# Kernel tuning notes

Hardware: AMD Instinct MI355X
Metric: run time of the kernel (lower is better)

Reference implementation:

```python
import jax, jax.numpy as jnp
import numpy as np

DIM = 1024; DEPTH = 6; HEADS = 16; DH = 64; NF = 16; VOCAB = 20000; B = 4; N = 1024
INNER = HEADS * DH
FF_INNER = int(DIM * 4 * 2 / 3)  # GEGLU inner dim = 2730


def _ln(x, g):
    # torch F.layer_norm with beta=0 buffer, eps=1e-5
    m = x.mean(-1, keepdims=True)
    v = ((x - m) ** 2).mean(-1, keepdims=True)
    return (x - m) / jnp.sqrt(v + 1e-5) * g


def _attn(x, ctx, mask, ln_g, Wq, Wkv, Wo):
    # faithful: LayerNorm applied to x (queries); context, if given, used raw for k/v
    xn = _ln(x, ln_g)
    kv_x = xn if ctx is None else ctx
    b, i, _ = x.shape
    j = kv_x.shape[1]
    q = (xn @ Wq).reshape(b, i, HEADS, DH) * (DH ** -0.5)
    k, v = jnp.split(kv_x @ Wkv, 2, axis=-1)
    k = k.reshape(b, j, HEADS, DH)
    v = v.reshape(b, j, HEADS, DH)
    sim = jnp.einsum('bihd,bjhd->bhij', q, k)
    sim = jnp.where(mask, sim, -jnp.finfo(sim.dtype).max)
    attn = jax.nn.softmax(sim, axis=-1)
    out = jnp.einsum('bhij,bjhd->bihd', attn, v).reshape(b, i, INNER)
    return out @ Wo


def _closs(a, b, ls):
    # CLIP-style ContrastiveLossWithTemperature
    an = a / jnp.linalg.norm(a, axis=-1, keepdims=True)
    bn = b / jnp.linalg.norm(b, axis=-1, keepdims=True)
    logits = jnp.exp(ls) * (an @ bn.T)
    lab = jnp.arange(a.shape[0])
    la = -jax.nn.log_softmax(logits, axis=-1)[lab, lab].mean()
    lb = -jax.nn.log_softmax(logits.T, axis=-1)[lab, lab].mean()
    return (la + lb) * 0.5


def setup_inputs() -> dict:
    key = jax.random.key(0)
    ks = jax.random.split(key, 16)
    rn = lambda k, s: jax.random.normal(k, s, jnp.float32) * 0.02
    return {
        'spliced_data': jax.random.normal(ks[0], (B, N), jnp.float32),
        'spliced_index': jax.random.randint(ks[1], (B, N), 0, VOCAB),
        'emb': rn(ks[2], (VOCAB, DIM)),
        'fusion_tokens': jax.random.normal(ks[3], (NF, DIM), jnp.float32),
        'return_tokens': jax.random.normal(ks[4], (2, DIM), jnp.float32),
        'ln1_g': jnp.ones((DEPTH, DIM), jnp.float32),
        'Wq': rn(ks[5], (DEPTH, DIM, INNER)),
        'Wkv': rn(ks[6], (DEPTH, DIM, 2 * INNER)),
        'Wo': rn(ks[7], (DEPTH, INNER, DIM)),
        'ln2_g': jnp.ones((DEPTH, DIM), jnp.float32),
        'Wff1': rn(ks[8], (DEPTH, DIM, 2 * FF_INNER)),
        'Wff2': rn(ks[9], (DEPTH, FF_INNER, DIM)),
        'norm_g': jnp.ones((DIM,), jnp.float32),
        'pool_ln_g': jnp.ones((DIM,), jnp.float32),
        'pWq': rn(ks[10], (DIM, INNER)),
        'pWkv': rn(ks[11], (DIM, 2 * INNER)),
        'pWo': rn(ks[12], (INNER, DIM)),
        'logit_scale_c': jnp.float32(np.log(1.0 / 0.07)),
        'logit_scale_f': jnp.float32(np.log(1.0 / 0.07)),
    }


def reference(spliced_data, spliced_index, emb, fusion_tokens, return_tokens,
              ln1_g, Wq, Wkv, Wo, ln2_g, Wff1, Wff2, norm_g,
              pool_ln_g, pWq, pWkv, pWo, logit_scale_c, logit_scale_f):
    b = spliced_data.shape[0]
    # BioZorroEncoder: value-weighted embedding lookup
    spliced_tokens = emb[spliced_index] * spliced_data[..., None]  # [b, N, DIM]
    tokens = jnp.concatenate(
        [spliced_tokens, jnp.broadcast_to(fusion_tokens, (b, NF, DIM))], axis=1)
    tt = jnp.concatenate([jnp.zeros((N,), jnp.int32), jnp.ones((NF,), jnp.int32)])
    # spliced attends spliced; fusion attends everything
    zmask = (tt[:, None] == tt[None, :]) | (tt[:, None] == 1)

    def body(t, p):
        l1, wq, wkv, wo, l2, w1, w2 = p
        t = _attn(t, None, zmask, l1, wq, wkv, wo) + t
        h = _ln(t, l2) @ w1
        xh, gate = jnp.split(h, 2, axis=-1)
        t = (jax.nn.gelu(gate, approximate=False) * xh) @ w2 + t
        return t, None

    tokens, _ = jax.lax.scan(body, tokens, (ln1_g, Wq, Wkv, Wo, ln2_g, Wff1, Wff2))
    tokens = _ln(tokens, norm_g)

    rtt = jnp.array([0, 1], jnp.int32)
    pm0 = rtt[:, None] == tt[None, :]
    # faithful to source operator precedence: (pm0 | rtt) == GLOBAL(2) -> all False
    pm = (pm0.astype(jnp.int32) | rtt[:, None]) == 2

    ret = jnp.broadcast_to(return_tokens, (b, 2, DIM))
    pooled = _attn(ret, tokens, pm, pool_ln_g, pWq, pWkv, pWo) + ret

    spliced = pooled[:, 0]
    fusion = pooled[:, 1]
    loss = _closs(spliced, spliced, logit_scale_c) + _closs(spliced, fusion, logit_scale_f)
    return loss
```

## Files before the change

kernel.cpp:

```cpp
#include <hip/hip_runtime.h>

typedef unsigned short u16;
typedef unsigned long long u64;
typedef __attribute__((ext_vector_type(8))) short short8;
typedef __attribute__((ext_vector_type(4))) float f32x4;

__device__ __forceinline__ u16 f2b(float f) {
  union { float f; unsigned u; } x; x.f = f;
  unsigned r = x.u + 0x7fffu + ((x.u >> 16) & 1u);
  return (u16)(r >> 16);
}
__device__ __forceinline__ float b2f(u16 h) {
  union { unsigned u; float f; } x; x.u = ((unsigned)h) << 16;
  return x.f;
}
__device__ __forceinline__ void gld16(const void* g, void* l) {
  __builtin_amdgcn_global_load_lds(
      (__attribute__((address_space(1))) const void*)g,
      (__attribute__((address_space(3))) void*)l, 16, 0, 0);
}

__global__ __launch_bounds__(256) void embed_k(
    const float* __restrict__ data, const int* __restrict__ idx,
    const float* __restrict__ emb, const float* __restrict__ fus,
    float* __restrict__ t) {
  int row = blockIdx.x;
  int b = row / 1040, n = row % 1040;
  int tid = threadIdx.x;
  const float4* src;
  float sc = 1.f;
  if (n < 1024) {
    int e = idx[b * 1024 + n];
    sc = data[b * 1024 + n];
    src = (const float4*)(emb + (long)e * 1024);
  } else {
    src = (const float4*)(fus + (long)(n - 1024) * 1024);
  }
  float4 v = src[tid];
  v.x *= sc; v.y *= sc; v.z *= sc; v.w *= sc;
  ((float4*)(t + (long)row * 1024))[tid] = v;
}

__global__ __launch_bounds__(256) void wtrans5_k(
    const float* __restrict__ sWq, const float* __restrict__ sWkv,
    const float* __restrict__ sWo, const float* __restrict__ sW1,
    const float* __restrict__ sW2,
    u16* __restrict__ dQkvT, u16* __restrict__ dWoT,
    u16* __restrict__ dF1T, u16* __restrict__ dF2T) {
  int id = blockIdx.x;
  const float* src; u16* dst; int K, N, Kpad, nx; float sc = 1.f;
  if (id < 1024)       { src = sWq;  dst = dQkvT;             K = 1024; N = 1024; Kpad = 1024; nx = 32; sc = 0.125f; }
  else if (id < 3072)  { id -= 1024; src = sWkv; dst = dQkvT + 1024 * 1024; K = 1024; N = 2048; Kpad = 1024; nx = 64; }
  else if (id < 4096)  { id -= 3072; src = sWo;  dst = dWoT;  K = 1024; N = 1024; Kpad = 1024; nx = 32; }
  else if (id < 9600)  { id -= 4096; src = sW1;  dst = dF1T;  K = 1024; N = 5460; Kpad = 1024; nx = 172; }
  else                 { id -= 9600; src = sW2;  dst = dF2T;  K = 2730; N = 1024; Kpad = 2752; nx = 32; }
  int n0 = (id % nx) * 32, k0 = (id / nx) * 32;
  __shared__ float tile[32][33];
  int x = threadIdx.x & 31, y = threadIdx.x >> 5;
#pragma unroll
  for (int i = 0; i < 4; i++) {
    int k = k0 + y + i * 8, n = n0 + x;
    tile[y + i * 8][x] = (k < K && n < N) ? src[(long)k * N + n] * sc : 0.f;
  }
  __syncthreads();
#pragma unroll
  for (int i = 0; i < 4; i++) {
    int n = n0 + y + i * 8, k = k0 + x;
    dst[(long)n * Kpad + k] = f2b(tile[x][y + i * 8]);
  }
}

__global__ __launch_bounds__(256) void ln_k(
    const float* __restrict__ t, const float* __restrict__ g,
    u16* __restrict__ xn) {
  int row = blockIdx.x, tid = threadIdx.x;
  int wave = tid >> 6, lane = tid & 63;
  float4 v = ((const float4*)(t + (long)row * 1024))[tid];
  float s = v.x + v.y + v.z + v.w;
#pragma unroll
  for (int o = 32; o > 0; o >>= 1) s += __shfl_xor(s, o, 64);
  __shared__ float r1[4], r2[4];
  if (lane == 0) r1[wave] = s;
  __syncthreads();
  float mean = (r1[0] + r1[1] + r1[2] + r1[3]) * (1.f / 1024.f);
  float dx = v.x - mean, dy = v.y - mean, dz = v.z - mean, dw = v.w - mean;
  float q = dx * dx + dy * dy + dz * dz + dw * dw;
#pragma unroll
  for (int o = 32; o > 0; o >>= 1) q += __shfl_xor(q, o, 64);
  if (lane == 0) r2[wave] = q;
  __syncthreads();
  float var = (r2[0] + r2[1] + r2[2] + r2[3]) * (1.f / 1024.f);
  float inv = rsqrtf(var + 1e-5f);
  float4 gv = ((const float4*)g)[tid];
  u64 pack = (u64)f2b(dx * inv * gv.x)
           | ((u64)f2b(dy * inv * gv.y) << 16)
           | ((u64)f2b(dz * inv * gv.z) << 32)
           | ((u64)f2b(dw * inv * gv.w) << 48);
  *(u64*)(xn + (long)row * 1024 + tid * 4) = pack;
}

__global__ __launch_bounds__(256) void lnred_k(
    float* __restrict__ t, const float* __restrict__ p0, const float* __restrict__ p1,
    const float* __restrict__ g, u16* __restrict__ xn) {
  int row = blockIdx.x, tid = threadIdx.x;
  int wave = tid >> 6, lane = tid & 63;
  long base = (long)row * 1024;
  float4 v = ((const float4*)(t + base))[tid];
  float4 a = ((const float4*)(p0 + base))[tid];
  float4 bq = ((const float4*)(p1 + base))[tid];
  v.x += a.x + bq.x; v.y += a.y + bq.y; v.z += a.z + bq.z; v.w += a.w + bq.w;
  ((float4*)(t + base))[tid] = v;
  float s = v.x + v.y + v.z + v.w;
#pragma unroll
  for (int o = 32; o > 0; o >>= 1) s += __shfl_xor(s, o, 64);
  __shared__ float r1[4], r2[4];
  if (lane == 0) r1[wave] = s;
  __syncthreads();
  float mean = (r1[0] + r1[1] + r1[2] + r1[3]) * (1.f / 1024.f);
  float dx = v.x - mean, dy = v.y - mean, dz = v.z - mean, dw = v.w - mean;
  float q = dx * dx + dy * dy + dz * dz + dw * dw;
#pragma unroll
  for (int o = 32; o > 0; o >>= 1) q += __shfl_xor(q, o, 64);
  if (lane == 0) r2[wave] = q;
  __syncthreads();
  float var = (r2[0] + r2[1] + r2[2] + r2[3]) * (1.f / 1024.f);
  float inv = rsqrtf(var + 1e-5f);
  float4 gv = ((const float4*)g)[tid];
  u64 pack = (u64)f2b(dx * inv * gv.x)
           | ((u64)f2b(dy * inv * gv.y) << 16)
           | ((u64)f2b(dz * inv * gv.z) << 32)
           | ((u64)f2b(dw * inv * gv.w) << 48);
  *(u64*)(xn + base + tid * 4) = pack;
}

__global__ __launch_bounds__(256) void redrow_k(
    float* __restrict__ t, const float* __restrict__ p0, const float* __restrict__ p1,
    float* __restrict__ rowm, float* __restrict__ rinv) {
  int row = blockIdx.x, tid = threadIdx.x;
  int wave = tid >> 6, lane = tid & 63;
  long base = (long)row * 1024;
  float4 v = ((const float4*)(t + base))[tid];
  float4 a = ((const float4*)(p0 + base))[tid];
  float4 bq = ((const float4*)(p1 + base))[tid];
  v.x += a.x + bq.x; v.y += a.y + bq.y; v.z += a.z + bq.z; v.w += a.w + bq.w;
  ((float4*)(t + base))[tid] = v;
  float s = v.x + v.y + v.z + v.w;
#pragma unroll
  for (int o = 32; o > 0; o >>= 1) s += __shfl_xor(s, o, 64);
  __shared__ float r1[4], r2[4];
  if (lane == 0) r1[wave] = s;
  __syncthreads();
  float mean = (r1[0] + r1[1] + r1[2] + r1[3]) * (1.f / 1024.f);
  float dx = v.x - mean, dy = v.y - mean, dz = v.z - mean, dw = v.w - mean;
  float q = dx * dx + dy * dy + dz * dz + dw * dw;
#pragma unroll
  for (int o = 32; o > 0; o >>= 1) q += __shfl_xor(q, o, 64);
  if (lane == 0) r2[wave] = q;
  __syncthreads();
  if (tid == 0) {
    float var = (r2[0] + r2[1] + r2[2] + r2[3]) * (1.f / 1024.f);
    rowm[row] = mean;
    rinv[row] = rsqrtf(var + 1e-5f);
  }
}

__global__ __launch_bounds__(256) void gemm_bt(
    const u16* __restrict__ A, int lda,
    const u16* __restrict__ Bt, int ldb,
    void* __restrict__ C, int ldc,
    int K, int mode, int gx, int ns, long pstride, u16* __restrict__ vt) {
  __shared__ u16 As[3][128 * 32];
  __shared__ u16 Bs[3][128 * 32];
  int tid = threadIdx.x;
  int wave = tid >> 6, lane = tid & 63;
  int col = lane & 15, grp = lane >> 4;
  int nwg = gridDim.x;
  int id = blockIdx.x;
  int q = nwg >> 3, r = nwg & 7;
  int xcd = id & 7, off = id >> 3;
  int wgid = (xcd < r ? xcd * (q + 1) : r * (q + 1) + (xcd - r) * q) + off;
  int tiles = nwg / ns;
  int ksp = wgid / tiles;
  int rem = wgid % tiles;
  int bm = rem % gx, bn = rem / gx;
  int nst = K >> 5;
  int k0 = ((nst * ksp) / ns) << 5;
  int k1 = ((nst * (ksp + 1)) / ns) << 5;
  int sr = wave * 16 + (lane >> 2);
  int sk = ((lane & 3) ^ ((lane >> 3) & 3)) * 8;
  const u16* aSrc = A + ((long)bm * 128 + sr) * lda + sk;
  const u16* bSrc = Bt + ((long)bn * 128 + sr) * ldb + sk;
  int wm = (wave >> 1) * 64, wn = (wave & 1) * 64;
  f32x4 acc[4][4] = {};

#define GSTAGE(buf, kt) do { \
    _Pragma("unroll") \
    for (int qq = 0; qq < 2; qq++) { \
      gld16(aSrc + (kt) + (long)qq * 64 * lda, &As[buf][wave * 512 + qq * 2048]); \
      gld16(bSrc + (kt) + (long)qq * 64 * ldb, &Bs[buf][wave * 512 + qq * 2048]); \
    } } while (0)

  GSTAGE(0, k0);
  if (k0 + 32 < k1) GSTAGE(1, k0 + 32);
  int cur = 0;
  int slot = (grp ^ ((col >> 1) & 3)) * 8;
  for (int kt = k0; kt < k1; kt += 32) {
    if (kt + 64 < k1) {
      int nb = cur + 2; if (nb >= 3) nb -= 3;
      GSTAGE(nb, kt + 64);
      asm volatile("s_waitcnt vmcnt(8)" ::: "memory");
    } else if (kt + 32 < k1) {
      asm volatile("s_waitcnt vmcnt(4)" ::: "memory");
    } else {
      asm volatile("s_waitcnt vmcnt(0)" ::: "memory");
    }
    __builtin_amdgcn_s_barrier();
    __builtin_amdgcn_sched_barrier(0);
    short8 af[4], bfv[4];
#pragma unroll
    for (int m = 0; m < 4; m++)
      af[m] = *(const short8*)&As[cur][(wm + m * 16 + col) * 32 + slot];
#pragma unroll
    for (int n = 0; n < 4; n++)
      bfv[n] = *(const short8*)&Bs[cur][(wn + n * 16 + col) * 32 + slot];
    __builtin_amdgcn_s_setprio(1);
#pragma unroll
    for (int m = 0; m < 4; m++)
#pragma unroll
      for (int n = 0; n < 4; n++)
        acc[m][n] = __builtin_amdgcn_mfma_f32_16x16x32_bf16(af[m], bfv[n], acc[m][n], 0, 0, 0);
    __builtin_amdgcn_s_setprio(0);
    __builtin_amdgcn_s_barrier();
    __builtin_amdgcn_sched_barrier(0);
    cur = (cur == 2) ? 0 : cur + 1;
  }
#undef GSTAGE
  long r0 = (long)bm * 128 + wm + grp * 4;
  int c0 = bn * 128 + wn + col;
  if (mode != 1) {
    u16* Cb = (u16*)C;
#pragma unroll
    for (int m = 0; m < 4; m++)
#pragma unroll
      for (int n = 0; n < 4; n++)
#pragma unroll
        for (int rr = 0; rr < 4; rr++)
          Cb[(r0 + m * 16 + rr) * ldc + c0 + n * 16] = f2b(acc[m][n][rr]);
    if (mode == 2 && bn >= 16) {
#pragma unroll
      for (int m = 0; m < 4; m++) {
        long row = r0 + m * 16;
        if (row < 4160) {
          int bidx = (int)(row / 1040);
          int j = (int)(row - (long)bidx * 1040);
#pragma unroll
          for (int n = 0; n < 4; n++) {
            int d = c0 + n * 16 - 2048;
            u64 pack = (u64)f2b(acc[m][n][0])
                     | ((u64)f2b(acc[m][n][1]) << 16)
                     | ((u64)f2b(acc[m][n][2]) << 32)
                     | ((u64)f2b(acc[m][n][3]) << 48);
            *(u64*)(vt + ((long)(bidx * 16 + (d >> 6)) * 64 + (d & 63)) * 1040 + j) = pack;
          }
        }
      }
    }
  } else {
    float* Cf = (float*)C + (long)ksp * pstride;
#pragma unroll
    for (int m = 0; m < 4; m++)
#pragma unroll
      for (int n = 0; n < 4; n++)
#pragma unroll
        for (int rr = 0; rr < 4; rr++)
          Cf[(r0 + m * 16 + rr) * ldc + c0 + n * 16] = acc[m][n][rr];
  }
}

__global__ __launch_bounds__(256) void attn_k(
    const u16* __restrict__ qkv, const u16* __restrict__ vt,
    u16* __restrict__ out) {
  int nwg = gridDim.x;
  int id = blockIdx.x;
  int q = nwg >> 3, r = nwg & 7;
  int xcd = id & 7, off = id >> 3;
  int wgid = (xcd < r ? xcd * (q + 1) : r * (q + 1) + (xcd - r) * q) + off;
  int bh = wgid / 17, it = wgid % 17;
  int b = bh >> 4, h = bh & 15;
  int tid = threadIdx.x, wave = tid >> 6, lane = tid & 63;
  int col = lane & 15, grp = lane >> 4;
  int i0 = it * 64;
  int jmax = (it == 16) ? 1040 : 1024;
  const u16* qb = qkv + (long)b * 1040 * 3072 + h * 64;
  const u16* kb = qkv + (long)b * 1040 * 3072 + 1024 + h * 64;
  const u16* vb = vt + (long)bh * 64 * 1040;
  __shared__ u16 Ks[2][64 * 64];
  __shared__ u16 Vs[2][64 * 64];
  __shared__ u16 Ps[4][16 * 64];

  int srow0 = wave * 8 + (lane >> 3);
  int gsw = ((lane & 7) ^ (srow0 & 7)) * 8;
#define ASTAGE(buf, j0s) do { \
    int jv = (j0s) + gsw; if (jv >= 1040) jv = 1032; \
    _Pragma("unroll") \
    for (int qq = 0; qq < 2; qq++) { \
      int rr = qq * 32 + srow0; \
      gld16(kb + (long)((j0s) + rr) * 3072 + gsw, &Ks[buf][qq * 2048 + wave * 512]); \
      gld16(vb + (long)rr * 1040 + jv, &Vs[buf][qq * 2048 + wave * 512]); \
    } } while (0)

  short8 aq[2];
  int qrow = i0 + wave * 16;
#pragma unroll
  for (int kf = 0; kf < 2; kf++)
    aq[kf] = *(const short8*)(qb + (long)(qrow + col) * 3072 + kf * 32 + grp * 8);

  short8 one8 = {};
  if (col == 0) {
#pragma unroll
    for (int i = 0; i < 8; i++) one8[i] = (short)0x3F80;
  }

  f32x4 oa[4] = {};
  f32x4 oa1 = {};

  ASTAGE(0, 0);
  int cur = 0;
  for (int j0 = 0; j0 < jmax; j0 += 64) {
    if (j0 + 64 < jmax) {
      ASTAGE(cur ^ 1, j0 + 64);
      asm volatile("s_waitcnt vmcnt(4)" ::: "memory");
    } else {
      asm volatile("s_waitcnt vmcnt(0)" ::: "memory");
    }
    __builtin_amdgcn_s_barrier();
    __builtin_amdgcn_sched_barrier(0);
    f32x4 s[4] = {};
#pragma unroll
    for (int kf = 0; kf < 2; kf++) {
      short8 bk[4];
#pragma unroll
      for (int n = 0; n < 4; n++) {
        int rk = n * 16 + col;
        bk[n] = *(const short8*)&Ks[cur][rk * 64 + ((kf * 32 + grp * 8) ^ ((rk & 7) << 3))];
      }
      __builtin_amdgcn_s_setprio(1);
#pragma unroll
      for (int n = 0; n < 4; n++)
        s[n] = __builtin_amdgcn_mfma_f32_16x16x32_bf16(aq[kf], bk[n], s[n], 0, 0, 0);
      __builtin_amdgcn_s_setprio(0);
    }
    if (j0 + 64 > jmax) {
      int lim = jmax - j0;
#pragma unroll
      for (int n = 0; n < 4; n++) {
        if (n * 16 + col >= lim) {
#pragma unroll
          for (int r2 = 0; r2 < 4; r2++) s[n][r2] = -1e30f;
        }
      }
    }
#pragma unroll
    for (int r2 = 0; r2 < 4; r2++) {
      int rp = grp * 4 + r2;
#pragma unroll
      for (int n = 0; n < 4; n++) {
        float p = __expf(s[n][r2]);
        Ps[wave][rp * 64 + ((n * 16 + col) ^ ((rp & 7) << 3))] = f2b(p);
      }
    }
#pragma unroll
    for (int kf = 0; kf < 2; kf++) {
      short8 ap, bv[4];
      int rm = col;
      ap = *(const short8*)&Ps[wave][rm * 64 + ((kf * 32 + grp * 8) ^ ((rm & 7) << 3))];
#pragma unroll
      for (int n = 0; n < 4; n++) {
        int rv = n * 16 + col;
        bv[n] = *(const short8*)&Vs[cur][rv * 64 + ((kf * 32 + grp * 8) ^ ((rv & 7) << 3))];
      }
      __builtin_amdgcn_s_setprio(1);
#pragma unroll
      for (int n = 0; n < 4; n++)
        oa[n] = __builtin_amdgcn_mfma_f32_16x16x32_bf16(ap, bv[n], oa[n], 0, 0, 0);
      oa1 = __builtin_amdgcn_mfma_f32_16x16x32_bf16(ap, one8, oa1, 0, 0, 0);
      __builtin_amdgcn_s_setprio(0);
    }
    __builtin_amdgcn_s_barrier();
    __builtin_amdgcn_sched_barrier(0);
    cur ^= 1;
  }
#undef ASTAGE
  float lr[4];
#pragma unroll
  for (int r2 = 0; r2 < 4; r2++) lr[r2] = __shfl(oa1[r2], lane & 48, 64);
#pragma unroll
  for (int n = 0; n < 4; n++)
#pragma unroll
    for (int r2 = 0; r2 < 4; r2++) {
      int i = i0 + wave * 16 + grp * 4 + r2;
      if (i < 1040)
        out[((long)b * 1040 + i) * 1024 + h * 64 + n * 16 + col] = f2b(oa[n][r2] / lr[r2]);
    }
}

__global__ __launch_bounds__(256) void act_k(
    const u16* __restrict__ h, u16* __restrict__ act) {
  int row = blockIdx.x;
  int c = blockIdx.y * 1024 + threadIdx.x * 4;
  if (c >= 2752) return;
  const u16* hr = h + (long)row * 5504;
  u64 xh4 = *(const u64*)(hr + c);
  unsigned g0 = *(const unsigned*)(hr + 2730 + c);
  unsigned g1 = *(const unsigned*)(hr + 2732 + c);
  u16 gv[4] = { (u16)g0, (u16)(g0 >> 16), (u16)g1, (u16)(g1 >> 16) };
  u64 pack = 0;
#pragma unroll
  for (int i = 0; i < 4; i++) {
    int cc = c + i;
    float r = 0.f;
    if (cc < 2730) {
      float xh = b2f((u16)(xh4 >> (16 * i)));
      float gt = b2f(gv[i]);
      float ge = 0.5f * gt * (1.f + erff(gt * 0.70710678118f));
      r = ge * xh;
    }
    pack |= ((u64)f2b(r)) << (16 * i);
  }
  *(u64*)(act + (long)row * 2752 + c) = pack;
}

__global__ __launch_bounds__(256) void wcolsum_k(
    const float* __restrict__ t, const float* __restrict__ rowm,
    const float* __restrict__ rinv, float* __restrict__ colsum,
    float* __restrict__ msum) {
  int b = blockIdx.x, c = blockIdx.y, tid = threadIdx.x;
  float a0 = 0, a1 = 0, a2 = 0, a3 = 0, ms = 0;
  for (int r = 0; r < 20; r++) {
    long row = (long)b * 1040 + c * 20 + r;
    float iv = rinv[row];
    float4 v = ((const float4*)(t + row * 1024))[tid];
    a0 += v.x * iv; a1 += v.y * iv; a2 += v.z * iv; a3 += v.w * iv;
    if (tid == 0) ms += rowm[row] * iv;
  }
  atomicAdd(&colsum[b * 1024 + tid * 4 + 0], a0);
  atomicAdd(&colsum[b * 1024 + tid * 4 + 1], a1);
  atomicAdd(&colsum[b * 1024 + tid * 4 + 2], a2);
  atomicAdd(&colsum[b * 1024 + tid * 4 + 3], a3);
  if (tid == 0) atomicAdd(&msum[b], ms);
}

__global__ __launch_bounds__(256) void mv1_k(
    const float* __restrict__ colsum, const float* __restrict__ msum,
    const float* __restrict__ g, const float* __restrict__ pWkv,
    float* __restrict__ tmp) {
  int b = blockIdx.x, n = blockIdx.y * 256 + threadIdx.x;
  float msb = msum[b];
  float acc = 0.f;
  for (int k = 0; k < 1024; k++) {
    float mk = g[k] * (colsum[b * 1024 + k] - msb);
    acc += mk * pWkv[(long)k * 2048 + 1024 + n];
  }
  tmp[b * 1024 + n] = acc * (1.f / 1040.f);
}

__global__ __launch_bounds__(256) void mv2_k(
    const float* __restrict__ tmp, const float* __restrict__ pWo,
    const float* __restrict__ ret, float* __restrict__ spl,
    float* __restrict__ fub) {
  int b = blockIdx.x, n = blockIdx.y * 256 + threadIdx.x;
  float acc = 0.f;
  for (int k = 0; k < 1024; k++) acc += tmp[b * 1024 + k] * pWo[(long)k * 1024 + n];
  spl[b * 1024 + n] = ret[n] + acc;
  fub[b * 1024 + n] = ret[1024 + n] + acc;
}

__device__ float closs_dev(const float L[4][4]) {
  float la = 0.f, lb = 0.f;
  for (int i = 0; i < 4; i++) {
    float mx = fmaxf(fmaxf(L[i][0], L[i][1]), fmaxf(L[i][2], L[i][3]));
    float sm = expf(L[i][0] - mx) + expf(L[i][1] - mx) + expf(L[i][2] - mx) + expf(L[i][3] - mx);
    la += mx + logf(sm) - L[i][i];
  }
  for (int j = 0; j < 4; j++) {
    float mx = fmaxf(fmaxf(L[0][j], L[1][j]), fmaxf(L[2][j], L[3][j]));
    float sm = expf(L[0][j] - mx) + expf(L[1][j] - mx) + expf(L[2][j] - mx) + expf(L[3][j] - mx);
    lb += mx + logf(sm) - L[j][j];
  }
  return 0.125f * (la + lb);
}

__global__ __launch_bounds__(256) void loss_k(
    const float* __restrict__ s, const float* __restrict__ f,
    const float* __restrict__ lsc, const float* __restrict__ lsf,
    float* __restrict__ out) {
  __shared__ float dots[36];
  int tid = threadIdx.x, wave = tid >> 6, lane = tid & 63;
  for (int d = wave; d < 36; d += 4) {
    const float *a, *bb;
    if (d < 16) { a = s + (d >> 2) * 1024; bb = s + (d & 3) * 1024; }
    else if (d < 32) { int e = d - 16; a = s + (e >> 2) * 1024; bb = f + (e & 3) * 1024; }
    else { a = f + (d - 32) * 1024; bb = a; }
    float p = 0.f;
    for (int k = lane; k < 1024; k += 64) p += a[k] * bb[k];
#pragma unroll
    for (int o = 32; o > 0; o >>= 1) p += __shfl_xor(p, o, 64);
    if (lane == 0) dots[d] = p;
  }
  __syncthreads();
  if (tid == 0) {
    float nS[4], nF[4];
    for (int i = 0; i < 4; i++) { nS[i] = sqrtf(dots[i * 4 + i]); nF[i] = sqrtf(dots[32 + i]); }
    float e1 = expf(lsc[0]), e2 = expf(lsf[0]);
    float L1[4][4], L2[4][4];
    for (int i = 0; i < 4; i++)
      for (int j = 0; j < 4; j++) {
        L1[i][j] = e1 * dots[i * 4 + j] / (nS[i] * nS[j]);
        L2[i][j] = e2 * dots[16 + i * 4 + j] / (nS[i] * nF[j]);
      }
    out[0] = closs_dev(L1) + closs_dev(L2);
  }
}

extern "C" void kernel_launch(void* const* d_in, const int* in_sizes, int n_in,
                              void* d_out, int out_size, void* d_ws, size_t ws_size,
                              hipStream_t stream) {
  (void)in_sizes; (void)n_in; (void)out_size; (void)ws_size;
  const float* sdata = (const float*)d_in[0];
  const int*   sidx  = (const int*)d_in[1];
  const float* emb   = (const float*)d_in[2];
  const float* fus   = (const float*)d_in[3];
  const float* ret   = (const float*)d_in[4];
  const float* ln1g  = (const float*)d_in[5];
  const float* Wq    = (const float*)d_in[6];
  const float* Wkv   = (const float*)d_in[7];
  const float* Wo    = (const float*)d_in[8];
  const float* ln2g  = (const float*)d_in[9];
  const float* Wff1  = (const float*)d_in[10];
  const float* Wff2  = (const float*)d_in[11];
  const float* normg = (const float*)d_in[12];
  const float* pWkv  = (const float*)d_in[15];
  const float* pWo   = (const float*)d_in[16];
  const float* lsc   = (const float*)d_in[17];
  const float* lsf   = (const float*)d_in[18];

  char* ws = (char*)d_ws;
  float* t   = (float*)(ws + 0L);
  u16* xn    = (u16*)(ws + 17301504L);
  char* U    = ws + 25952256L;
  u16* qkv   = (u16*)(U);
  u16* vtb   = (u16*)(U + 26738688L);
  u16* aout  = (u16*)(U + 35270656L);
  u16* hb    = (u16*)(U);
  u16* ab    = (u16*)(U + 46497792L);
  float* par0 = (float*)(U);
  float* par1 = (float*)(U + 17301504L);
  char* WT   = ws + 95698944L;
  u16* qkvT  = (u16*)(WT);
  u16* WoT   = (u16*)(WT + 6291456L);
  u16* f1T   = (u16*)(WT + 8388608L);
  u16* f2T   = (u16*)(WT + 19660800L);
  char* FIN  = ws + 120995840L;
  float* rowm   = (float*)(FIN);
  float* rinvp  = (float*)(FIN + 16640L);
  float* colsum = (float*)(FIN + 33280L);
  float* msum   = (float*)(FIN + 49664L);
  float* tmp    = (float*)(FIN + 49728L);
  float* spl    = (float*)(FIN + 66112L);
  float* fub    = (float*)(FIN + 82496L);
  const long PSTR = 4224L * 1024;

  embed_k<<<4160, 256, 0, stream>>>(sdata, sidx, emb, fus, t);

  for (int l = 0; l < 6; l++) {
    wtrans5_k<<<12352, 256, 0, stream>>>(
        Wq + (long)l * 1024 * 1024, Wkv + (long)l * 1024 * 2048,
        Wo + (long)l * 1024 * 1024, Wff1 + (long)l * 1024 * 5460,
        Wff2 + (long)l * 2730 * 1024, qkvT, WoT, f1T, f2T);

    if (l == 0)
      ln_k<<<4160, 256, 0, stream>>>(t, ln1g, xn);
    else
      lnred_k<<<4160, 256, 0, stream>>>(t, par0, par1, ln1g + l * 1024, xn);

    gemm_bt<<<33 * 24, 256, 0, stream>>>(xn, 1024, qkvT, 1024, qkv, 3072, 1024, 2, 33, 1, 0, vtb);
    attn_k<<<1088, 256, 0, stream>>>(qkv, vtb, aout);
    gemm_bt<<<33 * 8 * 2, 256, 0, stream>>>(aout, 1024, WoT, 1024, par0, 1024, 1024, 1, 33, 2, PSTR, vtb);
    lnred_k<<<4160, 256, 0, stream>>>(t, par0, par1, ln2g + l * 1024, xn);
    gemm_bt<<<33 * 43, 256, 0, stream>>>(xn, 1024, f1T, 1024, hb, 5504, 1024, 0, 33, 1, 0, vtb);
    act_k<<<dim3(4160, 3), 256, 0, stream>>>(hb, ab);
    gemm_bt<<<33 * 8 * 2, 256, 0, stream>>>(ab, 2752, f2T, 2752, par0, 1024, 2752, 1, 33, 2, PSTR, vtb);
  }

  redrow_k<<<4160, 256, 0, stream>>>(t, par0, par1, rowm, rinvp);
  hipMemsetAsync(colsum, 0, 16448, stream);
  wcolsum_k<<<dim3(4, 52), 256, 0, stream>>>(t, rowm, rinvp, colsum, msum);
  mv1_k<<<dim3(4, 4), 256, 0, stream>>>(colsum, msum, normg, pWkv, tmp);
  mv2_k<<<dim3(4, 4), 256, 0, stream>>>(tmp, pWo, ret, spl, fub);
  loss_k<<<1, 256, 0, stream>>>(spl, fub, lsc, lsf, (float*)d_out);
}
```

Before: 1.943 ms.

## Fuse GEGLU activation into FF1 GEMM epilogue via interleaved weight columns

Permutes the FF1 weight columns so each 32-column group interleaves 16 value columns with their 16 matching gate columns. The GEMM epilogue can then apply the exact-erf GELU gating and write the 2752-wide activation directly. This removes the separate act_k kernel and the round trip of the 5504-wide intermediate through global memory. In exchange the weight transpose uses a more complex gather index and the epilogue does erf work inside the GEMM.

```diff
diff --git a/kernel.cpp b/kernel.cpp
--- a/kernel.cpp
+++ b/kernel.cpp
@@ -48,11 +48,11 @@
     u16* __restrict__ dQkvT, u16* __restrict__ dWoT,
     u16* __restrict__ dF1T, u16* __restrict__ dF2T) {
   int id = blockIdx.x;
-  const float* src; u16* dst; int K, N, Kpad, nx; float sc = 1.f;
+  const float* src; u16* dst; int K, N, Kpad, nx; float sc = 1.f; int perm = 0;
   if (id < 1024)       { src = sWq;  dst = dQkvT;             K = 1024; N = 1024; Kpad = 1024; nx = 32; sc = 0.125f; }
   else if (id < 3072)  { id -= 1024; src = sWkv; dst = dQkvT + 1024 * 1024; K = 1024; N = 2048; Kpad = 1024; nx = 64; }
   else if (id < 4096)  { id -= 3072; src = sWo;  dst = dWoT;  K = 1024; N = 1024; Kpad = 1024; nx = 32; }
-  else if (id < 9600)  { id -= 4096; src = sW1;  dst = dF1T;  K = 1024; N = 5460; Kpad = 1024; nx = 172; }
+  else if (id < 9600)  { id -= 4096; src = sW1;  dst = dF1T;  K = 1024; N = 5504; Kpad = 1024; nx = 172; perm = 1; }
   else                 { id -= 9600; src = sW2;  dst = dF2T;  K = 2730; N = 1024; Kpad = 2752; nx = 32; }
   int n0 = (id % nx) * 32, k0 = (id / nx) * 32;
   __shared__ float tile[32][33];
@@ -60,7 +60,16 @@
 #pragma unroll
   for (int i = 0; i < 4; i++) {
     int k = k0 + y + i * 8, n = n0 + x;
-    tile[y + i * 8][x] = (k < K && n < N) ? src[(long)k * N + n] * sc : 0.f;
+    float val = 0.f;
+    if (perm) {
+      int p = n >> 5, sub = n & 31;
+      int o = (sub < 16) ? (p * 16 + sub) : (2714 + p * 16 + sub);
+      bool ok = (sub < 16) ? (o < 2730) : (o < 5460);
+      val = (k < K && ok) ? src[(long)k * 5460 + o] : 0.f;
+    } else {
+      val = (k < K && n < N) ? src[(long)k * N + n] * sc : 0.f;
+    }
+    tile[y + i * 8][x] = val;
   }
   __syncthreads();
 #pragma unroll
@@ -237,7 +246,24 @@
 #undef GSTAGE
   long r0 = (long)bm * 128 + wm + grp * 4;
   int c0 = bn * 128 + wn + col;
-  if (mode != 1) {
+  if (mode == 3) {
+    u16* Ab = (u16*)C;
+#pragma unroll
+    for (int m = 0; m < 4; m++)
+#pragma unroll
+      for (int np = 0; np < 2; np++) {
+        int ac = ((bn * 4 + (wn >> 5) + np) << 4) + col;
+#pragma unroll
+        for (int rr = 0; rr < 4; rr++) {
+          float xh = acc[m][np * 2][rr];
+          float gt = acc[m][np * 2 + 1][rr];
+          float rv = 0.f;
+          if (ac < 2730)
+            rv = 0.5f * gt * (1.f + erff(gt * 0.70710678118f)) * xh;
+          Ab[(r0 + m * 16 + rr) * ldc + ac] = f2b(rv);
+        }
+      }
+  } else if (mode != 1) {
     u16* Cb = (u16*)C;
 #pragma unroll
     for (int m = 0; m < 4; m++)
@@ -402,32 +428,6 @@
       if (i < 1040)
         out[((long)b * 1040 + i) * 1024 + h * 64 + n * 16 + col] = f2b(oa[n][r2] / lr[r2]);
     }
-}
-
-__global__ __launch_bounds__(256) void act_k(
-    const u16* __restrict__ h, u16* __restrict__ act) {
-  int row = blockIdx.x;
-  int c = blockIdx.y * 1024 + threadIdx.x * 4;
-  if (c >= 2752) return;
-  const u16* hr = h + (long)row * 5504;
-  u64 xh4 = *(const u64*)(hr + c);
-  unsigned g0 = *(const unsigned*)(hr + 2730 + c);
-  unsigned g1 = *(const unsigned*)(hr + 2732 + c);
-  u16 gv[4] = { (u16)g0, (u16)(g0 >> 16), (u16)g1, (u16)(g1 >> 16) };
-  u64 pack = 0;
-#pragma unroll
-  for (int i = 0; i < 4; i++) {
-    int cc = c + i;
-    float r = 0.f;
-    if (cc < 2730) {
-      float xh = b2f((u16)(xh4 >> (16 * i)));
-      float gt = b2f(gv[i]);
-      float ge = 0.5f * gt * (1.f + erff(gt * 0.70710678118f));
-      r = ge * xh;
-    }
-    pack |= ((u64)f2b(r)) << (16 * i);
-  }
-  *(u64*)(act + (long)row * 2752 + c) = pack;
 }
 
 __global__ __launch_bounds__(256) void wcolsum_k(
@@ -551,8 +551,7 @@
   u16* qkv   = (u16*)(U);
   u16* vtb   = (u16*)(U + 26738688L);
   u16* aout  = (u16*)(U + 35270656L);
-  u16* hb    = (u16*)(U);
-  u16* ab    = (u16*)(U + 46497792L);
+  u16* ab    = (u16*)(U + 35270656L);
   float* par0 = (float*)(U);
   float* par1 = (float*)(U + 17301504L);
   char* WT   = ws + 95698944L;
@@ -587,8 +586,7 @@
     attn_k<<<1088, 256, 0, stream>>>(qkv, vtb, aout);
     gemm_bt<<<33 * 8 * 2, 256, 0, stream>>>(aout, 1024, WoT, 1024, par0, 1024, 1024, 1, 33, 2, PSTR, vtb);
     lnred_k<<<4160, 256, 0, stream>>>(t, par0, par1, ln2g + l * 1024, xn);
-    gemm_bt<<<33 * 43, 256, 0, stream>>>(xn, 1024, f1T, 1024, hb, 5504, 1024, 0, 33, 1, 0, vtb);
-    act_k<<<dim3(4160, 3), 256, 0, stream>>>(hb, ab);
+    gemm_bt<<<33 * 43, 256, 0, stream>>>(xn, 1024, f1T, 1024, ab, 2752, 1024, 3, 33, 1, 0, vtb);
     gemm_bt<<<33 * 8 * 2, 256, 0, stream>>>(ab, 2752, f2T, 2752, par0, 1024, 2752, 1, 33, 2, PSTR, vtb);
   }
 
```

New measurement: 1.896 ms, median of 2. -2.4%, faster.
